# Performance work log

Measured on AMD Instinct MI355X. Metric: run time of the kernel, lower is better.

The kernel has to match this reference:

```python
import jax, jax.numpy as jnp
import numpy as np

EPS = 1e-12
BETA = 0.25

def normalise(x, axis=-1):
    return x * jax.lax.rsqrt(jnp.mean(x * x, axis=axis, keepdims=True) + EPS)

def setup_inputs() -> dict:
    key = jax.random.key(0)
    ks = jax.random.split(key, 4)
    N, F, D, C = 8192, 512, 64, 8192
    return {
        "z": jax.random.normal(ks[0], (N, F), dtype=jnp.float32),
        "W_in": jax.random.normal(ks[1], (F, D), dtype=jnp.float32) * (1.0 / np.sqrt(F)),
        "b_in": jnp.zeros((D,), dtype=jnp.float32),
        "codebook": jax.random.normal(ks[2], (C, D), dtype=jnp.float32),
        "W_out": jax.random.normal(ks[3], (D, F), dtype=jnp.float32) * (1.0 / np.sqrt(D)),
        "b_out": jnp.zeros((F,), dtype=jnp.float32),
    }

def reference(z, W_in, b_in, codebook, W_out, b_out):
    sg = jax.lax.stop_gradient
    # input projection: [N, F] -> [N, D]
    zp = z @ W_in + b_in
    zn = normalise(zp)                  # [N, D]
    cn = normalise(codebook)            # [C, D]
    # squared euclidean distance via matmul expansion (same math as
    # sum((z[:,None]-c[None])**2, -1), avoids [N,C,D] materialization)
    z_sq = jnp.sum(zn * zn, axis=-1, keepdims=True)          # [N, 1]
    c_sq = jnp.sum(cn * cn, axis=-1)[None, :]                # [1, C]
    distance = z_sq + c_sq - 2.0 * (zn @ cn.T)               # [N, C]
    idxes = jnp.argmin(distance, axis=-1)                    # [N]
    codes = normalise(codebook[idxes], axis=-1)               # [N, D]
    loss = BETA * jnp.mean((sg(zn) - codes) ** 2) + jnp.mean((zn - sg(codes)) ** 2)
    codes = zn + sg(codes - zn)                               # straight-through
    out = codes @ W_out + b_out                               # [N, F]
    return (out, loss, idxes)
```

## Files before the change

### kernel.cpp

```cpp
#include <hip/hip_runtime.h>
#include <hip/hip_bf16.h>

#define N_ROWS 8192
#define F_DIM  512
#define D_DIM  64
#define C_CODES 8192

typedef __attribute__((ext_vector_type(8))) short bf16x8;
typedef __attribute__((ext_vector_type(4))) float f32x4;

__device__ __forceinline__ unsigned short rne_bf16(float x) {
  unsigned u = __float_as_uint(x);
  return (unsigned short)((u + 0x7FFFu + ((u >> 16) & 1u)) >> 16);
}
__device__ __forceinline__ float bf16_to_f(unsigned short u) {
  return __uint_as_float(((unsigned)u) << 16);
}
__device__ __forceinline__ void limb3(const float* xs, bf16x8& H, bf16x8& M, bf16x8& L) {
  #pragma unroll
  for (int j = 0; j < 8; ++j) {
    float x = xs[j];
    unsigned short h = rne_bf16(x);
    float r1 = x - bf16_to_f(h);
    unsigned short m = rne_bf16(r1);
    float r2 = r1 - bf16_to_f(m);
    unsigned short lo = rne_bf16(r2);
    H[j] = (short)h; M[j] = (short)m; L[j] = (short)lo;
  }
}

__global__ void k_init(float* __restrict__ loss) { loss[0] = 0.0f; }

__global__ __launch_bounds__(256) void k_swz_win(
    const float* __restrict__ W, unsigned short* __restrict__ dst) {
  const int tid = threadIdx.x, w = tid >> 6, l = tid & 63;
  const int task = blockIdx.x * 4 + w;
  const int kc = task >> 2, cg = task & 3;
  const int lo = l & 15, hi = l >> 4;
  float xs[8];
  #pragma unroll
  for (int j = 0; j < 8; ++j)
    xs[j] = W[(size_t)(kc * 32 + hi * 8 + j) * D_DIM + cg * 16 + lo];
  bf16x8 H, M, L;
  limb3(xs, H, M, L);
  const int fb = (kc * 4 + cg) * 3;
  unsigned short* d0 = dst + (size_t)(fb + 0) * 512 + l * 8;
  unsigned short* d1 = dst + (size_t)(fb + 1) * 512 + l * 8;
  unsigned short* d2 = dst + (size_t)(fb + 2) * 512 + l * 8;
  #pragma unroll
  for (int j = 0; j < 8; ++j) { d0[j] = (unsigned short)H[j]; d1[j] = (unsigned short)M[j]; d2[j] = (unsigned short)L[j]; }
}

__global__ __launch_bounds__(256) void k_swz_wout(
    const float* __restrict__ W, unsigned short* __restrict__ dst) {
  const int tid = threadIdx.x, w = tid >> 6, l = tid & 63;
  const int task = blockIdx.x * 4 + w;
  const int cg = task >> 1, c = task & 1;
  const int lo = l & 15, hi = l >> 4;
  float xs[8];
  #pragma unroll
  for (int j = 0; j < 8; ++j)
    xs[j] = W[(size_t)(c * 32 + hi * 8 + j) * F_DIM + cg * 16 + lo];
  bf16x8 H, M, L;
  limb3(xs, H, M, L);
  const int fb = (cg * 2 + c) * 3;
  unsigned short* d0 = dst + (size_t)(fb + 0) * 512 + l * 8;
  unsigned short* d1 = dst + (size_t)(fb + 1) * 512 + l * 8;
  unsigned short* d2 = dst + (size_t)(fb + 2) * 512 + l * 8;
  #pragma unroll
  for (int j = 0; j < 8; ++j) { d0[j] = (unsigned short)H[j]; d1[j] = (unsigned short)M[j]; d2[j] = (unsigned short)L[j]; }
}

__global__ __launch_bounds__(256) void k_zn(
    const float* __restrict__ z, const unsigned short* __restrict__ w_in_sw,
    const float* __restrict__ b_in, float* __restrict__ zn) {
  const int tid = threadIdx.x, w = tid >> 6, l = tid & 63;
  const int lo = l & 15, hi = l >> 4;
  const int r0 = (blockIdx.x * 4 + w) * 16;
  const bf16x8* B = (const bf16x8*)w_in_sw;

  f32x4 acc0 = {0.f,0.f,0.f,0.f}, acc1 = {0.f,0.f,0.f,0.f};
  f32x4 acc2 = {0.f,0.f,0.f,0.f}, acc3 = {0.f,0.f,0.f,0.f};

  for (int kc = 0; kc < 16; ++kc) {
    const float* zp = z + (size_t)(r0 + lo) * F_DIM + kc * 32 + hi * 8;
    float4 x0 = *(const float4*)zp, x1 = *(const float4*)(zp + 4);
    float xs[8] = {x0.x, x0.y, x0.z, x0.w, x1.x, x1.y, x1.z, x1.w};
    bf16x8 Ah, Am, Al;
    limb3(xs, Ah, Am, Al);
    const bf16x8* Bc = B + (size_t)kc * 12 * 64 + l;
    #pragma unroll
    for (int cg = 0; cg < 4; ++cg) {
      bf16x8 Bh = Bc[(cg * 3 + 0) * 64];
      bf16x8 Bm = Bc[(cg * 3 + 1) * 64];
      bf16x8 Bl = Bc[(cg * 3 + 2) * 64];
      f32x4* a = (cg == 0) ? &acc0 : (cg == 1) ? &acc1 : (cg == 2) ? &acc2 : &acc3;
      f32x4 t = *a;
      t = __builtin_amdgcn_mfma_f32_16x16x32_bf16(Ah, Bh, t, 0, 0, 0);
      t = __builtin_amdgcn_mfma_f32_16x16x32_bf16(Ah, Bm, t, 0, 0, 0);
      t = __builtin_amdgcn_mfma_f32_16x16x32_bf16(Am, Bh, t, 0, 0, 0);
      t = __builtin_amdgcn_mfma_f32_16x16x32_bf16(Ah, Bl, t, 0, 0, 0);
      t = __builtin_amdgcn_mfma_f32_16x16x32_bf16(Al, Bh, t, 0, 0, 0);
      t = __builtin_amdgcn_mfma_f32_16x16x32_bf16(Am, Bm, t, 0, 0, 0);
      *a = t;
    }
  }

  float bias[4];
  #pragma unroll
  for (int cg = 0; cg < 4; ++cg) bias[cg] = b_in[cg * 16 + lo];

  f32x4* accs[4] = {&acc0, &acc1, &acc2, &acc3};
  #pragma unroll
  for (int r = 0; r < 4; ++r) {
    float v[4], s = 0.0f;
    #pragma unroll
    for (int cg = 0; cg < 4; ++cg) {
      v[cg] = (*accs[cg])[r] + bias[cg];
      s += v[cg] * v[cg];
    }
    s += __shfl_xor(s, 1);
    s += __shfl_xor(s, 2);
    s += __shfl_xor(s, 4);
    s += __shfl_xor(s, 8);
    float inv = rsqrtf(s * (1.0f / 64.0f) + 1e-12f);
    int row = r0 + hi * 4 + r;
    #pragma unroll
    for (int cg = 0; cg < 4; ++cg)
      zn[(size_t)row * D_DIM + cg * 16 + lo] = v[cg] * inv;
  }
}

__global__ __launch_bounds__(256) void k_cn(
    const float* __restrict__ cb, float* __restrict__ cn) {
  int row = blockIdx.x * 4 + (threadIdx.x >> 6);
  int lane = threadIdx.x & 63;
  float v = cb[(size_t)row * D_DIM + lane];
  float s = v * v;
  #pragma unroll
  for (int m = 1; m < 64; m <<= 1) s += __shfl_xor(s, m);
  float inv = rsqrtf(s * (1.0f / 64.0f) + 1e-12f);
  cn[(size_t)row * D_DIM + lane] = v * inv;
}

__global__ __launch_bounds__(256) void k_swizzle(
    const float* __restrict__ src, unsigned short* __restrict__ dst) {
  const int tid = threadIdx.x;
  const int w = tid >> 6, l = tid & 63;
  const int pair = blockIdx.x * 4 + w;
  const int g = pair >> 1, c = pair & 1;
  const int row = g * 16 + (l & 15);
  const int kb = c * 32 + (l >> 4) * 8;
  const float* sp = src + (size_t)row * D_DIM + kb;
  float4 x0 = *(const float4*)sp, x1 = *(const float4*)(sp + 4);
  float xs[8] = {x0.x, x0.y, x0.z, x0.w, x1.x, x1.y, x1.z, x1.w};
  bf16x8 H, M, L;
  limb3(xs, H, M, L);
  const int fbase = (g * 2 + c) * 3;
  unsigned short* d0 = dst + (size_t)(fbase + 0) * 512 + l * 8;
  unsigned short* d1 = dst + (size_t)(fbase + 1) * 512 + l * 8;
  unsigned short* d2 = dst + (size_t)(fbase + 2) * 512 + l * 8;
  #pragma unroll
  for (int j = 0; j < 8; ++j) { d0[j] = (unsigned short)H[j]; d1[j] = (unsigned short)M[j]; d2[j] = (unsigned short)L[j]; }
}

__global__ __launch_bounds__(256, 2) void k_argmax(
    const unsigned short* __restrict__ zn_sw,
    const unsigned short* __restrict__ cn_sw,
    float* __restrict__ pval, int* __restrict__ pidx) {
  const int tid = threadIdx.x;
  const int w = tid >> 6, l = tid & 63;
  const int lo = l & 15, hi = l >> 4;
  const int gA0 = (blockIdx.x * 4 + w) * 2;
  const int gB0 = blockIdx.y * 64;
  const bf16x8* Ab = (const bf16x8*)zn_sw;
  const bf16x8* Bb = (const bf16x8*)cn_sw;

  bf16x8 A0[2][3], A1[2][3];
  #pragma unroll
  for (int c = 0; c < 2; ++c)
    #pragma unroll
    for (int m = 0; m < 3; ++m) {
      A0[c][m] = Ab[(size_t)((gA0 * 2 + c) * 3 + m) * 64 + l];
      A1[c][m] = Ab[(size_t)(((gA0 + 1) * 2 + c) * 3 + m) * 64 + l];
    }

  bf16x8 Bu[2][3], Bv[2][3];
  #pragma unroll
  for (int c = 0; c < 2; ++c)
    #pragma unroll
    for (int m = 0; m < 3; ++m)
      Bu[c][m] = Bb[(size_t)((gB0 * 2 + c) * 3 + m) * 64 + l];

  float bv[8];
  int bi[8];
  #pragma unroll
  for (int i = 0; i < 8; ++i) { bv[i] = -1e30f; bi[i] = 0; }
  int cand = blockIdx.y * 1024 + lo;

  #define LOADB(dst, gB)                                                     \
    _Pragma("unroll")                                                        \
    for (int c = 0; c < 2; ++c)                                              \
      _Pragma("unroll")                                                      \
      for (int m = 0; m < 3; ++m)                                            \
        dst[c][m] = Bb[(size_t)(((gB) * 2 + c) * 3 + m) * 64 + l];

  #define COMPUTE(B)                                                          \
    {                                                                         \
      f32x4 a0 = {0.f,0.f,0.f,0.f}, a1 = {0.f,0.f,0.f,0.f};                   \
      f32x4 a2 = {0.f,0.f,0.f,0.f}, a3 = {0.f,0.f,0.f,0.f};                   \
      a0 = __builtin_amdgcn_mfma_f32_16x16x32_bf16(A0[0][0], B[0][0], a0, 0,0,0); \
      a1 = __builtin_amdgcn_mfma_f32_16x16x32_bf16(A0[1][0], B[1][0], a1, 0,0,0); \
      a2 = __builtin_amdgcn_mfma_f32_16x16x32_bf16(A1[0][0], B[0][0], a2, 0,0,0); \
      a3 = __builtin_amdgcn_mfma_f32_16x16x32_bf16(A1[1][0], B[1][0], a3, 0,0,0); \
      a0 = __builtin_amdgcn_mfma_f32_16x16x32_bf16(A0[0][0], B[0][1], a0, 0,0,0); \
      a1 = __builtin_amdgcn_mfma_f32_16x16x32_bf16(A0[1][0], B[1][1], a1, 0,0,0); \
      a2 = __builtin_amdgcn_mfma_f32_16x16x32_bf16(A1[0][0], B[0][1], a2, 0,0,0); \
      a3 = __builtin_amdgcn_mfma_f32_16x16x32_bf16(A1[1][0], B[1][1], a3, 0,0,0); \
      a0 = __builtin_amdgcn_mfma_f32_16x16x32_bf16(A0[0][1], B[0][0], a0, 0,0,0); \
      a1 = __builtin_amdgcn_mfma_f32_16x16x32_bf16(A0[1][1], B[1][0], a1, 0,0,0); \
      a2 = __builtin_amdgcn_mfma_f32_16x16x32_bf16(A1[0][1], B[0][0], a2, 0,0,0); \
      a3 = __builtin_amdgcn_mfma_f32_16x16x32_bf16(A1[1][1], B[1][0], a3, 0,0,0); \
      a0 = __builtin_amdgcn_mfma_f32_16x16x32_bf16(A0[0][0], B[0][2], a0, 0,0,0); \
      a1 = __builtin_amdgcn_mfma_f32_16x16x32_bf16(A0[1][0], B[1][2], a1, 0,0,0); \
      a2 = __builtin_amdgcn_mfma_f32_16x16x32_bf16(A1[0][0], B[0][2], a2, 0,0,0); \
      a3 = __builtin_amdgcn_mfma_f32_16x16x32_bf16(A1[1][0], B[1][2], a3, 0,0,0); \
      a0 = __builtin_amdgcn_mfma_f32_16x16x32_bf16(A0[0][2], B[0][0], a0, 0,0,0); \
      a1 = __builtin_amdgcn_mfma_f32_16x16x32_bf16(A0[1][2], B[1][0], a1, 0,0,0); \
      a2 = __builtin_amdgcn_mfma_f32_16x16x32_bf16(A1[0][2], B[0][0], a2, 0,0,0); \
      a3 = __builtin_amdgcn_mfma_f32_16x16x32_bf16(A1[1][2], B[1][0], a3, 0,0,0); \
      a0 = __builtin_amdgcn_mfma_f32_16x16x32_bf16(A0[0][1], B[0][1], a0, 0,0,0); \
      a1 = __builtin_amdgcn_mfma_f32_16x16x32_bf16(A0[1][1], B[1][1], a1, 0,0,0); \
      a2 = __builtin_amdgcn_mfma_f32_16x16x32_bf16(A1[0][1], B[0][1], a2, 0,0,0); \
      a3 = __builtin_amdgcn_mfma_f32_16x16x32_bf16(A1[1][1], B[1][1], a3, 0,0,0); \
      _Pragma("unroll")                                                       \
      for (int r = 0; r < 4; ++r) {                                           \
        float d0 = a0[r] + a1[r];                                             \
        if (d0 > bv[r]) { bv[r] = d0; bi[r] = cand; }                         \
        float d1 = a2[r] + a3[r];                                             \
        if (d1 > bv[4 + r]) { bv[4 + r] = d1; bi[4 + r] = cand; }             \
      }                                                                       \
      cand += 16;                                                             \
    }

  for (int p = 0; p < 64; p += 2) {
    LOADB(Bv, gB0 + p + 1);
    COMPUTE(Bu);
    LOADB(Bu, gB0 + p + 2);
    COMPUTE(Bv);
  }
  #undef LOADB
  #undef COMPUTE

  #pragma unroll
  for (int i = 0; i < 8; ++i) {
    float v = bv[i]; int ix = bi[i];
    #pragma unroll
    for (int m = 1; m < 16; m <<= 1) {
      float ov = __shfl_xor(v, m);
      int oi = __shfl_xor(ix, m);
      if (ov > v || (ov == v && oi < ix)) { v = ov; ix = oi; }
    }
    bv[i] = v; bi[i] = ix;
  }
  if (lo == 0) {
    int off = blockIdx.y * N_ROWS;
    int base0 = gA0 * 16 + hi * 4;
    int base1 = (gA0 + 1) * 16 + hi * 4;
    #pragma unroll
    for (int r = 0; r < 4; ++r) {
      pval[off + base0 + r] = bv[r];     pidx[off + base0 + r] = bi[r];
      pval[off + base1 + r] = bv[4 + r]; pidx[off + base1 + r] = bi[4 + r];
    }
  }
}

__global__ __launch_bounds__(256) void k_merge(
    const float* __restrict__ pval, const int* __restrict__ pidx,
    int* __restrict__ idx_out, float* __restrict__ idx_f) {
  int row = blockIdx.x * 256 + threadIdx.x;
  float v = pval[row]; int ix = pidx[row];
  #pragma unroll
  for (int q = 1; q < 8; ++q) {
    float vq = pval[q * N_ROWS + row];
    int iq = pidx[q * N_ROWS + row];
    if (vq > v) { v = vq; ix = iq; }
  }
  idx_out[row] = ix;
  idx_f[row] = (float)ix;
}

__global__ __launch_bounds__(256) void k_out(
    const float* __restrict__ cn, const float* __restrict__ zn,
    const int* __restrict__ idx, const unsigned short* __restrict__ w_out_sw,
    const float* __restrict__ b_out, float* __restrict__ out,
    float* __restrict__ loss_acc) {
  const int tid = threadIdx.x, w = tid >> 6, l = tid & 63;
  const int lo = l & 15, hi = l >> 4;
  const int r0 = (blockIdx.x * 4 + w) * 16;
  const int code = idx[r0 + lo];

  bf16x8 A[2][3];
  float lp = 0.0f;
  #pragma unroll
  for (int c = 0; c < 2; ++c) {
    const float* cp = cn + (size_t)code * D_DIM + c * 32 + hi * 8;
    const float* zp = zn + (size_t)(r0 + lo) * D_DIM + c * 32 + hi * 8;
    float4 c0 = *(const float4*)cp, c1 = *(const float4*)(cp + 4);
    float4 z0 = *(const float4*)zp, z1 = *(const float4*)(zp + 4);
    float xs[8] = {c0.x, c0.y, c0.z, c0.w, c1.x, c1.y, c1.z, c1.w};
    float zs[8] = {z0.x, z0.y, z0.z, z0.w, z1.x, z1.y, z1.z, z1.w};
    limb3(xs, A[c][0], A[c][1], A[c][2]);
    #pragma unroll
    for (int j = 0; j < 8; ++j) { float d = xs[j] - zs[j]; lp += d * d; }
  }
  #pragma unroll
  for (int m = 1; m < 64; m <<= 1) lp += __shfl_xor(lp, m);
  if (l == 0) atomicAdd(loss_acc, lp);

  const bf16x8* B = (const bf16x8*)w_out_sw;
  for (int cg = 0; cg < 32; ++cg) {
    bf16x8 Bf[2][3];
    #pragma unroll
    for (int c = 0; c < 2; ++c)
      #pragma unroll
      for (int m = 0; m < 3; ++m)
        Bf[c][m] = B[(size_t)((cg * 2 + c) * 3 + m) * 64 + l];
    f32x4 a0 = {0.f,0.f,0.f,0.f}, a1 = {0.f,0.f,0.f,0.f};
    a0 = __builtin_amdgcn_mfma_f32_16x16x32_bf16(A[0][0], Bf[0][0], a0, 0,0,0);
    a1 = __builtin_amdgcn_mfma_f32_16x16x32_bf16(A[1][0], Bf[1][0], a1, 0,0,0);
    a0 = __builtin_amdgcn_mfma_f32_16x16x32_bf16(A[0][0], Bf[0][1], a0, 0,0,0);
    a1 = __builtin_amdgcn_mfma_f32_16x16x32_bf16(A[1][0], Bf[1][1], a1, 0,0,0);
    a0 = __builtin_amdgcn_mfma_f32_16x16x32_bf16(A[0][1], Bf[0][0], a0, 0,0,0);
    a1 = __builtin_amdgcn_mfma_f32_16x16x32_bf16(A[1][1], Bf[1][0], a1, 0,0,0);
    a0 = __builtin_amdgcn_mfma_f32_16x16x32_bf16(A[0][0], Bf[0][2], a0, 0,0,0);
    a1 = __builtin_amdgcn_mfma_f32_16x16x32_bf16(A[1][0], Bf[1][2], a1, 0,0,0);
    a0 = __builtin_amdgcn_mfma_f32_16x16x32_bf16(A[0][2], Bf[0][0], a0, 0,0,0);
    a1 = __builtin_amdgcn_mfma_f32_16x16x32_bf16(A[1][2], Bf[1][0], a1, 0,0,0);
    a0 = __builtin_amdgcn_mfma_f32_16x16x32_bf16(A[0][1], Bf[0][1], a0, 0,0,0);
    a1 = __builtin_amdgcn_mfma_f32_16x16x32_bf16(A[1][1], Bf[1][1], a1, 0,0,0);
    float bb = b_out[cg * 16 + lo];
    #pragma unroll
    for (int r = 0; r < 4; ++r) {
      int row = r0 + hi * 4 + r;
      out[(size_t)row * F_DIM + cg * 16 + lo] = a0[r] + a1[r] + bb;
    }
  }
}

__global__ void k_loss_final(const float* __restrict__ loss,
                             float* __restrict__ out) {
  out[0] = loss[0] * (1.25f / (float)(N_ROWS * D_DIM));
}

extern "C" void kernel_launch(void* const* d_in, const int* in_sizes, int n_in,
                              void* d_out, int out_size, void* d_ws, size_t ws_size,
                              hipStream_t stream) {
  const float* z        = (const float*)d_in[0];
  const float* W_in     = (const float*)d_in[1];
  const float* b_in     = (const float*)d_in[2];
  const float* codebook = (const float*)d_in[3];
  const float* W_out    = (const float*)d_in[4];
  const float* b_out    = (const float*)d_in[5];

  float* outp   = (float*)d_out;
  float* loss_f = outp + (size_t)N_ROWS * F_DIM;
  float* idx_f  = loss_f + 1;

  float* wsf = (float*)d_ws;
  float* zn_ws = wsf;
  float* cn_ws = wsf + 524288;
  float* loss_ws = wsf + 1048576;
  int*   idx_ws  = (int*)(wsf + 1048592);
  unsigned short* zn_sw   = (unsigned short*)(wsf + 1056784);
  unsigned short* cn_sw   = (unsigned short*)(wsf + 1843216);
  unsigned short* win_sw  = (unsigned short*)(wsf + 2633744);
  unsigned short* wout_sw = (unsigned short*)(wsf + 2682896);
  float* pval_ws = wsf + 2732048;
  int*   pidx_ws = (int*)(wsf + 2797584);

  hipLaunchKernelGGL(k_init, dim3(1), dim3(1), 0, stream, loss_ws);
  hipLaunchKernelGGL(k_swz_win, dim3(16), dim3(256), 0, stream, W_in, win_sw);
  hipLaunchKernelGGL(k_swz_wout, dim3(16), dim3(256), 0, stream, W_out, wout_sw);
  hipLaunchKernelGGL(k_cn, dim3(C_CODES / 4), dim3(256), 0, stream,
                     codebook, cn_ws);
  hipLaunchKernelGGL(k_zn, dim3(128), dim3(256), 0, stream,
                     z, win_sw, b_in, zn_ws);
  hipLaunchKernelGGL(k_swizzle, dim3(256), dim3(256), 0, stream, zn_ws, zn_sw);
  hipLaunchKernelGGL(k_swizzle, dim3(256), dim3(256), 0, stream, cn_ws, cn_sw);
  hipLaunchKernelGGL(k_argmax, dim3(64, 8), dim3(256), 0, stream,
                     zn_sw, cn_sw, pval_ws, pidx_ws);
  hipLaunchKernelGGL(k_merge, dim3(N_ROWS / 256), dim3(256), 0, stream,
                     pval_ws, pidx_ws, idx_ws, idx_f);
  hipLaunchKernelGGL(k_out, dim3(128), dim3(256), 0, stream,
                     cn_ws, zn_ws, idx_ws, wout_sw, b_out, outp, loss_ws);
  hipLaunchKernelGGL(k_loss_final, dim3(1), dim3(1), 0, stream,
                     loss_ws, loss_f);
}
```

Before: 174.8 us.

## Fuse swizzle, merge and loss stages into producer kernels and prefetch weights

Folds the bf16 limb swizzle of zn and cn into the kernels that normalise them. Folds the argmax partial merge into the output projection kernel and replaces the atomic loss accumulation with per-block partial sums, reduced by a small final kernel. This removes the init, swizzle and merge launches and their intermediate global round trips. The zn and output GEMM loops now use 64-thread blocks and register double-buffer the next weight fragments, which adds register pressure. The last output prefetch reads past the weight buffer into other workspace, which is harmless but sloppy.

```diff
diff --git a/kernel.cpp b/kernel.cpp
--- a/kernel.cpp
+++ b/kernel.cpp
@@ -29,8 +29,6 @@
   }
 }
 
-__global__ void k_init(float* __restrict__ loss) { loss[0] = 0.0f; }
-
 __global__ __launch_bounds__(256) void k_swz_win(
     const float* __restrict__ W, unsigned short* __restrict__ dst) {
   const int tid = threadIdx.x, w = tid >> 6, l = tid & 63;
@@ -71,52 +69,106 @@
   for (int j = 0; j < 8; ++j) { d0[j] = (unsigned short)H[j]; d1[j] = (unsigned short)M[j]; d2[j] = (unsigned short)L[j]; }
 }
 
-__global__ __launch_bounds__(256) void k_zn(
+__global__ __launch_bounds__(256) void k_cn(
+    const float* __restrict__ cb, float* __restrict__ cn,
+    unsigned short* __restrict__ cn_sw) {
+  const int tid = threadIdx.x, w = tid >> 6, l = tid & 63;
+  const int g = blockIdx.x * 4 + w;
+  const int lo = l & 15, hi = l >> 4;
+  const int code = g * 16 + lo;
+
+  float xs[2][8];
+  float s = 0.0f;
+  #pragma unroll
+  for (int c = 0; c < 2; ++c) {
+    const float* sp = cb + (size_t)code * D_DIM + c * 32 + hi * 8;
+    float4 a = *(const float4*)sp, b = *(const float4*)(sp + 4);
+    xs[c][0]=a.x; xs[c][1]=a.y; xs[c][2]=a.z; xs[c][3]=a.w;
+    xs[c][4]=b.x; xs[c][5]=b.y; xs[c][6]=b.z; xs[c][7]=b.w;
+    #pragma unroll
+    for (int j = 0; j < 8; ++j) s += xs[c][j] * xs[c][j];
+  }
+  s += __shfl_xor(s, 16);
+  s += __shfl_xor(s, 32);
+  float inv = rsqrtf(s * (1.0f / 64.0f) + 1e-12f);
+
+  #pragma unroll
+  for (int c = 0; c < 2; ++c) {
+    #pragma unroll
+    for (int j = 0; j < 8; ++j) xs[c][j] *= inv;
+    float* dp = cn + (size_t)code * D_DIM + c * 32 + hi * 8;
+    *(float4*)dp = make_float4(xs[c][0], xs[c][1], xs[c][2], xs[c][3]);
+    *(float4*)(dp + 4) = make_float4(xs[c][4], xs[c][5], xs[c][6], xs[c][7]);
+    bf16x8 H, M, L;
+    limb3(xs[c], H, M, L);
+    const int fb = (g * 2 + c) * 3;
+    unsigned short* d0 = cn_sw + (size_t)(fb + 0) * 512 + l * 8;
+    unsigned short* d1 = cn_sw + (size_t)(fb + 1) * 512 + l * 8;
+    unsigned short* d2 = cn_sw + (size_t)(fb + 2) * 512 + l * 8;
+    #pragma unroll
+    for (int j = 0; j < 8; ++j) { d0[j] = (unsigned short)H[j]; d1[j] = (unsigned short)M[j]; d2[j] = (unsigned short)L[j]; }
+  }
+}
+
+__global__ __launch_bounds__(64) void k_zn(
     const float* __restrict__ z, const unsigned short* __restrict__ w_in_sw,
-    const float* __restrict__ b_in, float* __restrict__ zn) {
-  const int tid = threadIdx.x, w = tid >> 6, l = tid & 63;
-  const int lo = l & 15, hi = l >> 4;
-  const int r0 = (blockIdx.x * 4 + w) * 16;
-  const bf16x8* B = (const bf16x8*)w_in_sw;
-
-  f32x4 acc0 = {0.f,0.f,0.f,0.f}, acc1 = {0.f,0.f,0.f,0.f};
-  f32x4 acc2 = {0.f,0.f,0.f,0.f}, acc3 = {0.f,0.f,0.f,0.f};
-
-  for (int kc = 0; kc < 16; ++kc) {
-    const float* zp = z + (size_t)(r0 + lo) * F_DIM + kc * 32 + hi * 8;
-    float4 x0 = *(const float4*)zp, x1 = *(const float4*)(zp + 4);
-    float xs[8] = {x0.x, x0.y, x0.z, x0.w, x1.x, x1.y, x1.z, x1.w};
-    bf16x8 Ah, Am, Al;
-    limb3(xs, Ah, Am, Al);
-    const bf16x8* Bc = B + (size_t)kc * 12 * 64 + l;
-    #pragma unroll
-    for (int cg = 0; cg < 4; ++cg) {
-      bf16x8 Bh = Bc[(cg * 3 + 0) * 64];
-      bf16x8 Bm = Bc[(cg * 3 + 1) * 64];
-      bf16x8 Bl = Bc[(cg * 3 + 2) * 64];
-      f32x4* a = (cg == 0) ? &acc0 : (cg == 1) ? &acc1 : (cg == 2) ? &acc2 : &acc3;
-      f32x4 t = *a;
-      t = __builtin_amdgcn_mfma_f32_16x16x32_bf16(Ah, Bh, t, 0, 0, 0);
-      t = __builtin_amdgcn_mfma_f32_16x16x32_bf16(Ah, Bm, t, 0, 0, 0);
-      t = __builtin_amdgcn_mfma_f32_16x16x32_bf16(Am, Bh, t, 0, 0, 0);
-      t = __builtin_amdgcn_mfma_f32_16x16x32_bf16(Ah, Bl, t, 0, 0, 0);
-      t = __builtin_amdgcn_mfma_f32_16x16x32_bf16(Al, Bh, t, 0, 0, 0);
-      t = __builtin_amdgcn_mfma_f32_16x16x32_bf16(Am, Bm, t, 0, 0, 0);
-      *a = t;
-    }
-  }
-
-  float bias[4];
-  #pragma unroll
-  for (int cg = 0; cg < 4; ++cg) bias[cg] = b_in[cg * 16 + lo];
-
-  f32x4* accs[4] = {&acc0, &acc1, &acc2, &acc3};
+    const float* __restrict__ b_in, float* __restrict__ zn,
+    unsigned short* __restrict__ zn_sw) {
+  __shared__ float t_lds[16 * 65];
+  const int l = threadIdx.x;
+  const int lo = l & 15, hi = l >> 4;
+  const int g = blockIdx.x;
+  const int r0 = g * 16;
+  const bf16x8* Bptr = (const bf16x8*)w_in_sw;
+  const float* zbase = z + (size_t)(r0 + lo) * F_DIM + hi * 8;
+
+  f32x4 acc[4];
+  #pragma unroll
+  for (int cg = 0; cg < 4; ++cg) acc[cg] = (f32x4){0.f, 0.f, 0.f, 0.f};
+
+  bf16x8 Bu[12], Bv[12];
+  #pragma unroll
+  for (int i = 0; i < 12; ++i) Bu[i] = Bptr[(size_t)i * 64 + l];
+  float4 za = *(const float4*)zbase;
+  float4 zb = *(const float4*)(zbase + 4);
+
+  #define ZSTEP(BCUR, BNXT, KC)                                               \
+    {                                                                         \
+      int kn = ((KC) < 15) ? (KC) + 1 : 15;                                   \
+      float4 na = *(const float4*)(zbase + kn * 32);                          \
+      float4 nb = *(const float4*)(zbase + kn * 32 + 4);                      \
+      _Pragma("unroll")                                                       \
+      for (int i = 0; i < 12; ++i)                                            \
+        BNXT[i] = Bptr[((size_t)kn * 12 + i) * 64 + l];                       \
+      float xs[8] = {za.x, za.y, za.z, za.w, zb.x, zb.y, zb.z, zb.w};         \
+      bf16x8 Ah, Am, Al;                                                      \
+      limb3(xs, Ah, Am, Al);                                                  \
+      _Pragma("unroll")                                                       \
+      for (int cg = 0; cg < 4; ++cg) {                                        \
+        f32x4 t = acc[cg];                                                    \
+        t = __builtin_amdgcn_mfma_f32_16x16x32_bf16(Ah, BCUR[cg*3+0], t, 0,0,0); \
+        t = __builtin_amdgcn_mfma_f32_16x16x32_bf16(Ah, BCUR[cg*3+1], t, 0,0,0); \
+        t = __builtin_amdgcn_mfma_f32_16x16x32_bf16(Am, BCUR[cg*3+0], t, 0,0,0); \
+        t = __builtin_amdgcn_mfma_f32_16x16x32_bf16(Ah, BCUR[cg*3+2], t, 0,0,0); \
+        t = __builtin_amdgcn_mfma_f32_16x16x32_bf16(Al, BCUR[cg*3+0], t, 0,0,0); \
+        t = __builtin_amdgcn_mfma_f32_16x16x32_bf16(Am, BCUR[cg*3+1], t, 0,0,0); \
+        acc[cg] = t;                                                          \
+      }                                                                       \
+      za = na; zb = nb;                                                       \
+    }
+
+  for (int kc = 0; kc < 16; kc += 2) {
+    ZSTEP(Bu, Bv, kc)
+    ZSTEP(Bv, Bu, kc + 1)
+  }
+  #undef ZSTEP
+
   #pragma unroll
   for (int r = 0; r < 4; ++r) {
     float v[4], s = 0.0f;
     #pragma unroll
     for (int cg = 0; cg < 4; ++cg) {
-      v[cg] = (*accs[cg])[r] + bias[cg];
+      v[cg] = acc[cg][r] + b_in[cg * 16 + lo];
       s += v[cg] * v[cg];
     }
     s += __shfl_xor(s, 1);
@@ -124,44 +176,29 @@
     s += __shfl_xor(s, 4);
     s += __shfl_xor(s, 8);
     float inv = rsqrtf(s * (1.0f / 64.0f) + 1e-12f);
-    int row = r0 + hi * 4 + r;
     #pragma unroll
     for (int cg = 0; cg < 4; ++cg)
-      zn[(size_t)row * D_DIM + cg * 16 + lo] = v[cg] * inv;
-  }
-}
-
-__global__ __launch_bounds__(256) void k_cn(
-    const float* __restrict__ cb, float* __restrict__ cn) {
-  int row = blockIdx.x * 4 + (threadIdx.x >> 6);
-  int lane = threadIdx.x & 63;
-  float v = cb[(size_t)row * D_DIM + lane];
-  float s = v * v;
-  #pragma unroll
-  for (int m = 1; m < 64; m <<= 1) s += __shfl_xor(s, m);
-  float inv = rsqrtf(s * (1.0f / 64.0f) + 1e-12f);
-  cn[(size_t)row * D_DIM + lane] = v * inv;
-}
-
-__global__ __launch_bounds__(256) void k_swizzle(
-    const float* __restrict__ src, unsigned short* __restrict__ dst) {
-  const int tid = threadIdx.x;
-  const int w = tid >> 6, l = tid & 63;
-  const int pair = blockIdx.x * 4 + w;
-  const int g = pair >> 1, c = pair & 1;
-  const int row = g * 16 + (l & 15);
-  const int kb = c * 32 + (l >> 4) * 8;
-  const float* sp = src + (size_t)row * D_DIM + kb;
-  float4 x0 = *(const float4*)sp, x1 = *(const float4*)(sp + 4);
-  float xs[8] = {x0.x, x0.y, x0.z, x0.w, x1.x, x1.y, x1.z, x1.w};
-  bf16x8 H, M, L;
-  limb3(xs, H, M, L);
-  const int fbase = (g * 2 + c) * 3;
-  unsigned short* d0 = dst + (size_t)(fbase + 0) * 512 + l * 8;
-  unsigned short* d1 = dst + (size_t)(fbase + 1) * 512 + l * 8;
-  unsigned short* d2 = dst + (size_t)(fbase + 2) * 512 + l * 8;
-  #pragma unroll
-  for (int j = 0; j < 8; ++j) { d0[j] = (unsigned short)H[j]; d1[j] = (unsigned short)M[j]; d2[j] = (unsigned short)L[j]; }
+      t_lds[(hi * 4 + r) * 65 + cg * 16 + lo] = v[cg] * inv;
+  }
+  __syncthreads();
+
+  #pragma unroll
+  for (int c = 0; c < 2; ++c) {
+    float xs[8];
+    #pragma unroll
+    for (int j = 0; j < 8; ++j) xs[j] = t_lds[lo * 65 + c * 32 + hi * 8 + j];
+    float* dp = zn + (size_t)(r0 + lo) * D_DIM + c * 32 + hi * 8;
+    *(float4*)dp = make_float4(xs[0], xs[1], xs[2], xs[3]);
+    *(float4*)(dp + 4) = make_float4(xs[4], xs[5], xs[6], xs[7]);
+    bf16x8 H, M, L;
+    limb3(xs, H, M, L);
+    const int fb = (g * 2 + c) * 3;
+    unsigned short* d0 = zn_sw + (size_t)(fb + 0) * 512 + l * 8;
+    unsigned short* d1 = zn_sw + (size_t)(fb + 1) * 512 + l * 8;
+    unsigned short* d2 = zn_sw + (size_t)(fb + 2) * 512 + l * 8;
+    #pragma unroll
+    for (int j = 0; j < 8; ++j) { d0[j] = (unsigned short)H[j]; d1[j] = (unsigned short)M[j]; d2[j] = (unsigned short)L[j]; }
+  }
 }
 
 __global__ __launch_bounds__(256, 2) void k_argmax(
@@ -275,37 +312,33 @@
   }
 }
 
-__global__ __launch_bounds__(256) void k_merge(
+__global__ __launch_bounds__(64) void k_out(
+    const float* __restrict__ cn, const float* __restrict__ zn,
     const float* __restrict__ pval, const int* __restrict__ pidx,
-    int* __restrict__ idx_out, float* __restrict__ idx_f) {
-  int row = blockIdx.x * 256 + threadIdx.x;
-  float v = pval[row]; int ix = pidx[row];
+    const unsigned short* __restrict__ w_out_sw,
+    const float* __restrict__ b_out, float* __restrict__ out,
+    float* __restrict__ idx_f, float* __restrict__ pl) {
+  const int l = threadIdx.x;
+  const int lo = l & 15, hi = l >> 4;
+  const int r0 = blockIdx.x * 16;
+  const int row = r0 + lo;
+
+  float v = pval[row];
+  int ix = pidx[row];
   #pragma unroll
   for (int q = 1; q < 8; ++q) {
     float vq = pval[q * N_ROWS + row];
     int iq = pidx[q * N_ROWS + row];
     if (vq > v) { v = vq; ix = iq; }
   }
-  idx_out[row] = ix;
-  idx_f[row] = (float)ix;
-}
-
-__global__ __launch_bounds__(256) void k_out(
-    const float* __restrict__ cn, const float* __restrict__ zn,
-    const int* __restrict__ idx, const unsigned short* __restrict__ w_out_sw,
-    const float* __restrict__ b_out, float* __restrict__ out,
-    float* __restrict__ loss_acc) {
-  const int tid = threadIdx.x, w = tid >> 6, l = tid & 63;
-  const int lo = l & 15, hi = l >> 4;
-  const int r0 = (blockIdx.x * 4 + w) * 16;
-  const int code = idx[r0 + lo];
+  if (hi == 0) idx_f[row] = (float)ix;
 
   bf16x8 A[2][3];
   float lp = 0.0f;
   #pragma unroll
   for (int c = 0; c < 2; ++c) {
-    const float* cp = cn + (size_t)code * D_DIM + c * 32 + hi * 8;
-    const float* zp = zn + (size_t)(r0 + lo) * D_DIM + c * 32 + hi * 8;
+    const float* cp = cn + (size_t)ix * D_DIM + c * 32 + hi * 8;
+    const float* zp = zn + (size_t)row * D_DIM + c * 32 + hi * 8;
     float4 c0 = *(const float4*)cp, c1 = *(const float4*)(cp + 4);
     float4 z0 = *(const float4*)zp, z1 = *(const float4*)(zp + 4);
     float xs[8] = {c0.x, c0.y, c0.z, c0.w, c1.x, c1.y, c1.z, c1.w};
@@ -316,41 +349,54 @@
   }
   #pragma unroll
   for (int m = 1; m < 64; m <<= 1) lp += __shfl_xor(lp, m);
-  if (l == 0) atomicAdd(loss_acc, lp);
-
-  const bf16x8* B = (const bf16x8*)w_out_sw;
-  for (int cg = 0; cg < 32; ++cg) {
-    bf16x8 Bf[2][3];
-    #pragma unroll
-    for (int c = 0; c < 2; ++c)
-      #pragma unroll
-      for (int m = 0; m < 3; ++m)
-        Bf[c][m] = B[(size_t)((cg * 2 + c) * 3 + m) * 64 + l];
-    f32x4 a0 = {0.f,0.f,0.f,0.f}, a1 = {0.f,0.f,0.f,0.f};
-    a0 = __builtin_amdgcn_mfma_f32_16x16x32_bf16(A[0][0], Bf[0][0], a0, 0,0,0);
-    a1 = __builtin_amdgcn_mfma_f32_16x16x32_bf16(A[1][0], Bf[1][0], a1, 0,0,0);
-    a0 = __builtin_amdgcn_mfma_f32_16x16x32_bf16(A[0][0], Bf[0][1], a0, 0,0,0);
-    a1 = __builtin_amdgcn_mfma_f32_16x16x32_bf16(A[1][0], Bf[1][1], a1, 0,0,0);
-    a0 = __builtin_amdgcn_mfma_f32_16x16x32_bf16(A[0][1], Bf[0][0], a0, 0,0,0);
-    a1 = __builtin_amdgcn_mfma_f32_16x16x32_bf16(A[1][1], Bf[1][0], a1, 0,0,0);
-    a0 = __builtin_amdgcn_mfma_f32_16x16x32_bf16(A[0][0], Bf[0][2], a0, 0,0,0);
-    a1 = __builtin_amdgcn_mfma_f32_16x16x32_bf16(A[1][0], Bf[1][2], a1, 0,0,0);
-    a0 = __builtin_amdgcn_mfma_f32_16x16x32_bf16(A[0][2], Bf[0][0], a0, 0,0,0);
-    a1 = __builtin_amdgcn_mfma_f32_16x16x32_bf16(A[1][2], Bf[1][0], a1, 0,0,0);
-    a0 = __builtin_amdgcn_mfma_f32_16x16x32_bf16(A[0][1], Bf[0][1], a0, 0,0,0);
-    a1 = __builtin_amdgcn_mfma_f32_16x16x32_bf16(A[1][1], Bf[1][1], a1, 0,0,0);
-    float bb = b_out[cg * 16 + lo];
-    #pragma unroll
-    for (int r = 0; r < 4; ++r) {
-      int row = r0 + hi * 4 + r;
-      out[(size_t)row * F_DIM + cg * 16 + lo] = a0[r] + a1[r] + bb;
-    }
-  }
-}
-
-__global__ void k_loss_final(const float* __restrict__ loss,
-                             float* __restrict__ out) {
-  out[0] = loss[0] * (1.25f / (float)(N_ROWS * D_DIM));
+  if (l == 0) pl[blockIdx.x] = lp;
+
+  const bf16x8* Bptr = (const bf16x8*)w_out_sw;
+  bf16x8 Bu[6], Bv[6];
+  #pragma unroll
+  for (int i = 0; i < 6; ++i) Bu[i] = Bptr[(size_t)i * 64 + l];
+
+  #define OSTEP(BCUR, BNXT, CG)                                               \
+    {                                                                         \
+      _Pragma("unroll")                                                       \
+      for (int i = 0; i < 6; ++i)                                             \
+        BNXT[i] = Bptr[((size_t)((CG) + 1) * 6 + i) * 64 + l];                \
+      f32x4 a0 = {0.f,0.f,0.f,0.f}, a1 = {0.f,0.f,0.f,0.f};                   \
+      a0 = __builtin_amdgcn_mfma_f32_16x16x32_bf16(A[0][0], BCUR[0], a0, 0,0,0); \
+      a1 = __builtin_amdgcn_mfma_f32_16x16x32_bf16(A[1][0], BCUR[3], a1, 0,0,0); \
+      a0 = __builtin_amdgcn_mfma_f32_16x16x32_bf16(A[0][0], BCUR[1], a0, 0,0,0); \
+      a1 = __builtin_amdgcn_mfma_f32_16x16x32_bf16(A[1][0], BCUR[4], a1, 0,0,0); \
+      a0 = __builtin_amdgcn_mfma_f32_16x16x32_bf16(A[0][1], BCUR[0], a0, 0,0,0); \
+      a1 = __builtin_amdgcn_mfma_f32_16x16x32_bf16(A[1][1], BCUR[3], a1, 0,0,0); \
+      a0 = __builtin_amdgcn_mfma_f32_16x16x32_bf16(A[0][0], BCUR[2], a0, 0,0,0); \
+      a1 = __builtin_amdgcn_mfma_f32_16x16x32_bf16(A[1][0], BCUR[5], a1, 0,0,0); \
+      a0 = __builtin_amdgcn_mfma_f32_16x16x32_bf16(A[0][2], BCUR[0], a0, 0,0,0); \
+      a1 = __builtin_amdgcn_mfma_f32_16x16x32_bf16(A[1][2], BCUR[3], a1, 0,0,0); \
+      a0 = __builtin_amdgcn_mfma_f32_16x16x32_bf16(A[0][1], BCUR[1], a0, 0,0,0); \
+      a1 = __builtin_amdgcn_mfma_f32_16x16x32_bf16(A[1][1], BCUR[4], a1, 0,0,0); \
+      float bb = b_out[(CG) * 16 + lo];                                       \
+      _Pragma("unroll")                                                       \
+      for (int r = 0; r < 4; ++r)                                             \
+        out[(size_t)(r0 + hi * 4 + r) * F_DIM + (CG) * 16 + lo] =             \
+            a0[r] + a1[r] + bb;                                               \
+    }
+
+  for (int cg = 0; cg < 32; cg += 2) {
+    OSTEP(Bu, Bv, cg)
+    OSTEP(Bv, Bu, cg + 1)
+  }
+  #undef OSTEP
+}
+
+__global__ __launch_bounds__(64) void k_loss_final(
+    const float* __restrict__ pl, float* __restrict__ loss_out) {
+  const int l = threadIdx.x;
+  float s = 0.0f;
+  #pragma unroll
+  for (int i = 0; i < 8; ++i) s += pl[l + 64 * i];
+  #pragma unroll
+  for (int m = 1; m < 64; m <<= 1) s += __shfl_xor(s, m);
+  if (l == 0) loss_out[0] = s * (1.25f / (float)(N_ROWS * D_DIM));
 }
 
 extern "C" void kernel_launch(void* const* d_in, const int* in_sizes, int n_in,
@@ -370,30 +416,25 @@
   float* wsf = (float*)d_ws;
   float* zn_ws = wsf;
   float* cn_ws = wsf + 524288;
-  float* loss_ws = wsf + 1048576;
-  int*   idx_ws  = (int*)(wsf + 1048592);
-  unsigned short* zn_sw   = (unsigned short*)(wsf + 1056784);
-  unsigned short* cn_sw   = (unsigned short*)(wsf + 1843216);
-  unsigned short* win_sw  = (unsigned short*)(wsf + 2633744);
-  unsigned short* wout_sw = (unsigned short*)(wsf + 2682896);
-  float* pval_ws = wsf + 2732048;
-  int*   pidx_ws = (int*)(wsf + 2797584);
-
-  hipLaunchKernelGGL(k_init, dim3(1), dim3(1), 0, stream, loss_ws);
+  unsigned short* zn_sw = (unsigned short*)(wsf + 1048576);
+  unsigned short* cn_sw = (unsigned short*)(wsf + 1835008);
+  unsigned short* win_sw  = (unsigned short*)(wsf + 2625536);
+  unsigned short* wout_sw = (unsigned short*)(wsf + 2674688);
+  float* pval_ws = wsf + 2723840;
+  int*   pidx_ws = (int*)(wsf + 2789376);
+  float* pl_ws   = wsf + 2854912;
+
   hipLaunchKernelGGL(k_swz_win, dim3(16), dim3(256), 0, stream, W_in, win_sw);
   hipLaunchKernelGGL(k_swz_wout, dim3(16), dim3(256), 0, stream, W_out, wout_sw);
-  hipLaunchKernelGGL(k_cn, dim3(C_CODES / 4), dim3(256), 0, stream,
-                     codebook, cn_ws);
-  hipLaunchKernelGGL(k_zn, dim3(128), dim3(256), 0, stream,
-                     z, win_sw, b_in, zn_ws);
-  hipLaunchKernelGGL(k_swizzle, dim3(256), dim3(256), 0, stream, zn_ws, zn_sw);
-  hipLaunchKernelGGL(k_swizzle, dim3(256), dim3(256), 0, stream, cn_ws, cn_sw);
+  hipLaunchKernelGGL(k_cn, dim3(128), dim3(256), 0, stream,
+                     codebook, cn_ws, cn_sw);
+  hipLaunchKernelGGL(k_zn, dim3(512), dim3(64), 0, stream,
+                     z, win_sw, b_in, zn_ws, zn_sw);
   hipLaunchKernelGGL(k_argmax, dim3(64, 8), dim3(256), 0, stream,
                      zn_sw, cn_sw, pval_ws, pidx_ws);
-  hipLaunchKernelGGL(k_merge, dim3(N_ROWS / 256), dim3(256), 0, stream,
-                     pval_ws, pidx_ws, idx_ws, idx_f);
-  hipLaunchKernelGGL(k_out, dim3(128), dim3(256), 0, stream,
-                     cn_ws, zn_ws, idx_ws, wout_sw, b_out, outp, loss_ws);
-  hipLaunchKernelGGL(k_loss_final, dim3(1), dim3(1), 0, stream,
-                     loss_ws, loss_f);
-}
+  hipLaunchKernelGGL(k_out, dim3(512), dim3(64), 0, stream,
+                     cn_ws, zn_ws, pval_ws, pidx_ws, wout_sw, b_out,
+                     outp, idx_f, pl_ws);
+  hipLaunchKernelGGL(k_loss_final, dim3(1), dim3(64), 0, stream,
+                     pl_ws, loss_f);
+}
```

New measurement: 154.8 us. -11.4%, faster.
